# Kernel tuning notes

Measured on AMD Instinct MI355X. Metric: run time of the kernel, lower is better.

Reference implementation:

```python
import jax, jax.numpy as jnp
import numpy as np

L, C, S = 4096, 128, 64
SAMPLE_RATE = 4096.0  # Hz; dt offset is 1/sample_rate as in the flax module


def setup_inputs() -> dict:
    key = jax.random.key(0)
    ks = jax.random.split(key, 4)
    x = jax.random.normal(ks[0], (L, C), dtype=jnp.float32)
    # S4D-real init: A = -arange(1, S+1), param stores log(-A) broadcast to (C, S)
    A_log = jnp.broadcast_to(
        jnp.log(jnp.arange(1, S + 1, dtype=jnp.float32)), (C, S)
    )
    sc = 1.0 / np.sqrt(C)  # lecun_normal-like scale for Dense kernels
    B_kernel = (jax.random.normal(ks[1], (C, S)) * sc).astype(jnp.float32)
    B_bias = jnp.zeros((S,), jnp.float32)
    C_kernel = (jax.random.normal(ks[2], (C, S)) * sc).astype(jnp.float32)
    C_bias = jnp.zeros((S,), jnp.float32)
    dt_kernel = (jax.random.normal(ks[3], (C, C)) * sc).astype(jnp.float32)
    dt_bias = jnp.zeros((C,), jnp.float32)
    return {
        "x": x,
        "A_log": A_log,
        "B_kernel": B_kernel,
        "B_bias": B_bias,
        "C_kernel": C_kernel,
        "C_bias": C_bias,
        "dt_kernel": dt_kernel,
        "dt_bias": dt_bias,
    }


def reference(x, A_log, B_kernel, B_bias, C_kernel, C_bias, dt_kernel, dt_bias):
    # ssm params
    A = -jnp.exp(A_log)                                   # (C, S), negative real
    B = 1.0 + x @ B_kernel + B_bias                       # (L, S)
    Cm = x @ C_kernel + C_bias                            # (L, S)
    dt = jax.nn.softplus(1.0 / SAMPLE_RATE + x @ dt_kernel + dt_bias)  # (L, C)
    # discretization (ZOH for diagonal real A)
    At = jnp.exp(A[None, :, :] * dt[:, :, None])          # (L, C, S)
    ut = (At - 1.0) * (B[:, None, :] / A[None, :, :]) * x[:, :, None]  # (L, C, S)

    # parallel linear-recurrence scan: h_t = At_t * h_{t-1} + ut_t, h0 = 0
    def comb(e1, e2):
        a1, u1 = e1
        a2, u2 = e2
        return (a2 * a1, a2 * u1 + u2)

    _, ht = jax.lax.associative_scan(comb, (At, ut))      # scans over axis 0 (L)
    y = jnp.einsum("ls,lcs->lc", Cm, ht)                  # (L, C)
    return y
```

## Files before the change

### kernel.cpp

```cpp
#include <hip/hip_runtime.h>
#include <math.h>

#define LL 4096
#define CC 128
#define SS 64
#define CLEN 32
#define GW 8
#define NG 16
#define CS 8192

__global__ __launch_bounds__(256) void k_proj(
    const float* __restrict__ x,
    const float* __restrict__ Bk, const float* __restrict__ Bb,
    const float* __restrict__ Ck, const float* __restrict__ Cb,
    const float* __restrict__ Dk, const float* __restrict__ Db,
    float* __restrict__ Bmat, float* __restrict__ Cmat,
    float* __restrict__ DTmT, float* __restrict__ xT)
{
    __shared__ float xs[CC][20];
    const int r0 = blockIdx.x * 16;
    const int t = threadIdx.x;
    {
        const int r = t >> 4, k8 = (t & 15) * 8;
        const float4 v0 = *(const float4*)&x[(r0 + r) * CC + k8];
        const float4 v1 = *(const float4*)&x[(r0 + r) * CC + k8 + 4];
        xs[k8+0][r] = v0.x; xs[k8+1][r] = v0.y; xs[k8+2][r] = v0.z; xs[k8+3][r] = v0.w;
        xs[k8+4][r] = v1.x; xs[k8+5][r] = v1.y; xs[k8+6][r] = v1.z; xs[k8+7][r] = v1.w;
    }
    __syncthreads();
    {
        const int k = t >> 1, half = (t & 1) * 8;
        const float4 a = *(const float4*)&xs[k][half];
        const float4 b = *(const float4*)&xs[k][half + 4];
        *(float4*)&xT[k * LL + r0 + half]     = a;
        *(float4*)&xT[k * LL + r0 + half + 4] = b;
    }
    const int tc = t & 63, tr = t >> 6;
    const float* Wb; int wstride, wo;
    if (tc < 16)      { Wb = Bk; wstride = SS; wo = 4 * tc; }
    else if (tc < 32) { Wb = Ck; wstride = SS; wo = 4 * tc - 64; }
    else              { Wb = Dk; wstride = CC; wo = 4 * tc - 128; }
    float acc[4][4];
#pragma unroll
    for (int r = 0; r < 4; ++r)
#pragma unroll
        for (int j = 0; j < 4; ++j) acc[r][j] = 0.0f;
    for (int k = 0; k < CC; ++k) {
        const float4 wq = *(const float4*)(Wb + k * wstride + wo);
        const float4 xq = *(const float4*)&xs[k][4 * tr];
        const float wv[4] = {wq.x, wq.y, wq.z, wq.w};
        const float xv[4] = {xq.x, xq.y, xq.z, xq.w};
#pragma unroll
        for (int r = 0; r < 4; ++r)
#pragma unroll
            for (int j = 0; j < 4; ++j) acc[r][j] = fmaf(xv[r], wv[j], acc[r][j]);
    }
    const int rb = r0 + 4 * tr;
    if (tc < 32) {
        const float* bb = (tc < 16) ? Bb : Cb;
        const float add = (tc < 16) ? 1.0f : 0.0f;
        float bias[4];
#pragma unroll
        for (int j = 0; j < 4; ++j) bias[j] = add + bb[wo + j];
        float* dst = (tc < 16) ? Bmat : Cmat;
#pragma unroll
        for (int r = 0; r < 4; ++r) {
            const float4 o = make_float4(acc[r][0] + bias[0], acc[r][1] + bias[1],
                                         acc[r][2] + bias[2], acc[r][3] + bias[3]);
            *(float4*)&dst[(rb + r) * SS + wo] = o;
        }
    } else {
#pragma unroll
        for (int j = 0; j < 4; ++j) {
            const float bj = Db[wo + j] + 0.000244140625f;
            float sp[4];
#pragma unroll
            for (int r = 0; r < 4; ++r) {
                const float z = acc[r][j] + bj;
                sp[r] = fmaxf(z, 0.0f) + log1pf(__expf(-fabsf(z)));
            }
            *(float4*)&DTmT[(wo + j) * LL + rb] = make_float4(sp[0], sp[1], sp[2], sp[3]);
        }
    }
}

__global__ __launch_bounds__(512, 4) void k_sweep1(
    const float* __restrict__ xT, const float* __restrict__ A_log,
    const float* __restrict__ Bmat, const float* __restrict__ DTmT,
    float* __restrict__ Ga, float* __restrict__ Gu)
{
    __shared__ float2 agg[GW][SS];
    const int lane = threadIdx.x & 63;
    const int w = __builtin_amdgcn_readfirstlane(threadIdx.x >> 6);
    const int c = blockIdx.x >> 4;
    const int g = blockIdx.x & (NG - 1);
    const int j = c * SS + lane;
    const float A = -__expf(A_log[j]);
    const float invA = 1.0f / A;
    const int l0 = (g * GW + w) * CLEN;
    const float* dtp = DTmT + c * LL + l0;
    const float* xp  = xT   + c * LL + l0;
    const float* Bp  = Bmat + l0 * SS + lane;
    float ap = 1.0f, uc = 0.0f;
#pragma unroll
    for (int i = 0; i < CLEN; ++i) {
        const float At = __expf(A * dtp[i]);
        const float u  = (At - 1.0f) * invA * (Bp[i * SS] * xp[i]);
        ap *= At;
        uc = fmaf(At, uc, u);
    }
    agg[w][lane] = make_float2(ap, uc);
    __syncthreads();
    if (w == 0) {
        float ga = 1.0f, gu = 0.0f;
#pragma unroll
        for (int k = 0; k < GW; ++k) {
            const float2 t = agg[k][lane];
            gu = fmaf(t.x, gu, t.y);
            ga *= t.x;
        }
        Ga[g * CS + j] = ga;
        Gu[g * CS + j] = gu;
    }
}

__global__ __launch_bounds__(512, 4) void k_emit(
    const float* __restrict__ xT, const float* __restrict__ A_log,
    const float* __restrict__ Bmat, const float* __restrict__ Cmat,
    const float* __restrict__ DTmT,
    const float* __restrict__ Ga, const float* __restrict__ Gu,
    float* __restrict__ y)
{
    __shared__ float2 agg[GW][SS];
    const int lane = threadIdx.x & 63;
    const int w = __builtin_amdgcn_readfirstlane(threadIdx.x >> 6);
    const int c = blockIdx.x >> 4;
    const int g = blockIdx.x & (NG - 1);
    const int j = c * SS + lane;
    const float A = -__expf(A_log[j]);
    const float invA = 1.0f / A;
    float hg = 0.0f;
    {
        float gar[NG - 1], gur[NG - 1];
#pragma unroll
        for (int gg = 0; gg < NG - 1; ++gg) {
            gar[gg] = Ga[gg * CS + j];
            gur[gg] = Gu[gg * CS + j];
        }
#pragma unroll
        for (int gg = 0; gg < NG - 1; ++gg)
            hg = (gg < g) ? fmaf(gar[gg], hg, gur[gg]) : hg;
    }
    const int l0 = (g * GW + w) * CLEN;
    const float* dtp = DTmT + c * LL + l0;
    const float* xp  = xT   + c * LL + l0;
    const float* Bp  = Bmat + l0 * SS + lane;
    const float* Cp  = Cmat + l0 * SS + lane;
    float at[CLEN], uu[CLEN];
    {
        float ap = 1.0f, uc = 0.0f;
#pragma unroll
        for (int i = 0; i < CLEN; ++i) {
            at[i] = __expf(A * dtp[i]);
            uu[i] = (at[i] - 1.0f) * invA * (Bp[i * SS] * xp[i]);
            ap *= at[i];
            uc = fmaf(at[i], uc, uu[i]);
        }
        agg[w][lane] = make_float2(ap, uc);
    }
    __syncthreads();
    float ea = 1.0f, eu = 0.0f;
    for (int k = 0; k < w; ++k) {
        const float2 t = agg[k][lane];
        eu = fmaf(t.x, eu, t.y);
        ea *= t.x;
    }
    float h = fmaf(ea, hg, eu);
#pragma unroll
    for (int i = 0; i < CLEN; ++i) {
        h = fmaf(at[i], h, uu[i]);
        uu[i] = Cp[i * SS] * h;
    }
#pragma unroll
    for (int k = 0; k < 5; ++k) {
        const int d = 1 << k;
        const bool hi = (lane & d) != 0;
#pragma unroll
        for (int i2 = 0; i2 < (CLEN >> (k + 1)); ++i2) {
            const float a = uu[2 * i2], b = uu[2 * i2 + 1];
            const float send = hi ? a : b;
            const float t = __shfl_xor(send, d, 64);
            uu[i2] = (hi ? b : a) + t;
        }
    }
    const float t = __shfl_xor(uu[0], 32, 64);
    const float yv = uu[0] + t;
    if (lane < 32) y[(l0 + lane) * CC + c] = yv;
}

extern "C" void kernel_launch(void* const* d_in, const int* in_sizes, int n_in,
                              void* d_out, int out_size, void* d_ws, size_t ws_size,
                              hipStream_t stream)
{
    const float* x  = (const float*)d_in[0];
    const float* Al = (const float*)d_in[1];
    const float* Bk = (const float*)d_in[2];
    const float* Bb = (const float*)d_in[3];
    const float* Ck = (const float*)d_in[4];
    const float* Cb = (const float*)d_in[5];
    const float* Dk = (const float*)d_in[6];
    const float* Db = (const float*)d_in[7];
    float* y  = (float*)d_out;
    float* ws = (float*)d_ws;

    float* Bmat = ws;
    float* Cmat = Bmat + LL * SS;
    float* DTmT = Cmat + LL * SS;
    float* xT   = DTmT + CC * LL;
    float* Ga   = xT   + CC * LL;
    float* Gu   = Ga   + NG * CS;

    k_proj  <<<LL / 16, 256, 0, stream>>>(x, Bk, Bb, Ck, Cb, Dk, Db, Bmat, Cmat, DTmT, xT);
    k_sweep1<<<CC * NG, 512, 0, stream>>>(xT, Al, Bmat, DTmT, Ga, Gu);
    k_emit  <<<CC * NG, 512, 0, stream>>>(xT, Al, Bmat, Cmat, DTmT, Ga, Gu, y);
}
```

Before: 49.83 us.

## Split projection across twice the blocks, use exp2 and pack carry state

The projection kernel now launches twice as many blocks. Each row stripe is split so one block computes the dt projection plus the x transpose, and the other computes the B and C projections, each thread producing two columns instead of four. The scan kernels replace __expf with a hardware exp2 on a pre-scaled A, and store the group carries as interleaved float2 so each load is a single 8-byte access. This is meant to raise parallelism in the projection stage and trim transcendental and load instructions, at the cost of each stripe of x being staged into shared memory twice.

```diff
diff --git a/kernel.cpp b/kernel.cpp
--- a/kernel.cpp
+++ b/kernel.cpp
@@ -8,6 +8,7 @@
 #define GW 8
 #define NG 16
 #define CS 8192
+#define LOG2E 1.44269504088896f
 
 __global__ __launch_bounds__(256) void k_proj(
     const float* __restrict__ x,
@@ -18,7 +19,9 @@
     float* __restrict__ DTmT, float* __restrict__ xT)
 {
     __shared__ float xs[CC][20];
-    const int r0 = blockIdx.x * 16;
+    const int stripe = blockIdx.x >> 1;
+    const int half   = blockIdx.x & 1;
+    const int r0 = stripe * 16;
     const int t = threadIdx.x;
     {
         const int r = t >> 4, k8 = (t & 15) * 8;
@@ -28,58 +31,65 @@
         xs[k8+4][r] = v1.x; xs[k8+5][r] = v1.y; xs[k8+6][r] = v1.z; xs[k8+7][r] = v1.w;
     }
     __syncthreads();
-    {
-        const int k = t >> 1, half = (t & 1) * 8;
-        const float4 a = *(const float4*)&xs[k][half];
-        const float4 b = *(const float4*)&xs[k][half + 4];
-        *(float4*)&xT[k * LL + r0 + half]     = a;
-        *(float4*)&xT[k * LL + r0 + half + 4] = b;
-    }
     const int tc = t & 63, tr = t >> 6;
-    const float* Wb; int wstride, wo;
-    if (tc < 16)      { Wb = Bk; wstride = SS; wo = 4 * tc; }
-    else if (tc < 32) { Wb = Ck; wstride = SS; wo = 4 * tc - 64; }
-    else              { Wb = Dk; wstride = CC; wo = 4 * tc - 128; }
-    float acc[4][4];
-#pragma unroll
-    for (int r = 0; r < 4; ++r)
-#pragma unroll
-        for (int j = 0; j < 4; ++j) acc[r][j] = 0.0f;
-    for (int k = 0; k < CC; ++k) {
-        const float4 wq = *(const float4*)(Wb + k * wstride + wo);
-        const float4 xq = *(const float4*)&xs[k][4 * tr];
-        const float wv[4] = {wq.x, wq.y, wq.z, wq.w};
-        const float xv[4] = {xq.x, xq.y, xq.z, xq.w};
-#pragma unroll
-        for (int r = 0; r < 4; ++r)
-#pragma unroll
-            for (int j = 0; j < 4; ++j) acc[r][j] = fmaf(xv[r], wv[j], acc[r][j]);
-    }
+    const int c2 = 2 * tc;
     const int rb = r0 + 4 * tr;
-    if (tc < 32) {
-        const float* bb = (tc < 16) ? Bb : Cb;
-        const float add = (tc < 16) ? 1.0f : 0.0f;
-        float bias[4];
-#pragma unroll
-        for (int j = 0; j < 4; ++j) bias[j] = add + bb[wo + j];
-        float* dst = (tc < 16) ? Bmat : Cmat;
-#pragma unroll
-        for (int r = 0; r < 4; ++r) {
-            const float4 o = make_float4(acc[r][0] + bias[0], acc[r][1] + bias[1],
-                                         acc[r][2] + bias[2], acc[r][3] + bias[3]);
-            *(float4*)&dst[(rb + r) * SS + wo] = o;
-        }
-    } else {
-#pragma unroll
-        for (int j = 0; j < 4; ++j) {
-            const float bj = Db[wo + j] + 0.000244140625f;
+    if (half == 1) {
+        const int k = t >> 1, h8 = (t & 1) * 8;
+        const float4 a = *(const float4*)&xs[k][h8];
+        const float4 b = *(const float4*)&xs[k][h8 + 4];
+        *(float4*)&xT[k * LL + r0 + h8]     = a;
+        *(float4*)&xT[k * LL + r0 + h8 + 4] = b;
+        float acc[4][2];
+#pragma unroll
+        for (int r = 0; r < 4; ++r) { acc[r][0] = 0.f; acc[r][1] = 0.f; }
+        const float* W = Dk + c2;
+        for (int k2 = 0; k2 < CC; ++k2) {
+            const float2 wq = *(const float2*)(W + k2 * CC);
+            const float4 xq = *(const float4*)&xs[k2][4 * tr];
+            const float xv[4] = {xq.x, xq.y, xq.z, xq.w};
+#pragma unroll
+            for (int r = 0; r < 4; ++r) {
+                acc[r][0] = fmaf(xv[r], wq.x, acc[r][0]);
+                acc[r][1] = fmaf(xv[r], wq.y, acc[r][1]);
+            }
+        }
+#pragma unroll
+        for (int j = 0; j < 2; ++j) {
+            const float bj = Db[c2 + j] + 0.000244140625f;
             float sp[4];
 #pragma unroll
             for (int r = 0; r < 4; ++r) {
                 const float z = acc[r][j] + bj;
                 sp[r] = fmaxf(z, 0.0f) + log1pf(__expf(-fabsf(z)));
             }
-            *(float4*)&DTmT[(wo + j) * LL + rb] = make_float4(sp[0], sp[1], sp[2], sp[3]);
+            *(float4*)&DTmT[(c2 + j) * LL + rb] = make_float4(sp[0], sp[1], sp[2], sp[3]);
+        }
+    } else {
+        const bool isB = (c2 < 64);
+        const int wo = isB ? c2 : (c2 - 64);
+        const float* W = (isB ? Bk : Ck) + wo;
+        const float add = isB ? 1.0f : 0.0f;
+        const float* bb = isB ? Bb : Cb;
+        float* dst = isB ? Bmat : Cmat;
+        float acc[4][2];
+#pragma unroll
+        for (int r = 0; r < 4; ++r) { acc[r][0] = 0.f; acc[r][1] = 0.f; }
+        for (int k2 = 0; k2 < CC; ++k2) {
+            const float2 wq = *(const float2*)(W + k2 * SS);
+            const float4 xq = *(const float4*)&xs[k2][4 * tr];
+            const float xv[4] = {xq.x, xq.y, xq.z, xq.w};
+#pragma unroll
+            for (int r = 0; r < 4; ++r) {
+                acc[r][0] = fmaf(xv[r], wq.x, acc[r][0]);
+                acc[r][1] = fmaf(xv[r], wq.y, acc[r][1]);
+            }
+        }
+        const float b0 = add + bb[wo], b1 = add + bb[wo + 1];
+#pragma unroll
+        for (int r = 0; r < 4; ++r) {
+            const float2 o = make_float2(acc[r][0] + b0, acc[r][1] + b1);
+            *(float2*)&dst[(rb + r) * SS + wo] = o;
         }
     }
 }
@@ -87,7 +97,7 @@
 __global__ __launch_bounds__(512, 4) void k_sweep1(
     const float* __restrict__ xT, const float* __restrict__ A_log,
     const float* __restrict__ Bmat, const float* __restrict__ DTmT,
-    float* __restrict__ Ga, float* __restrict__ Gu)
+    float2* __restrict__ GaGu)
 {
     __shared__ float2 agg[GW][SS];
     const int lane = threadIdx.x & 63;
@@ -96,6 +106,7 @@
     const int g = blockIdx.x & (NG - 1);
     const int j = c * SS + lane;
     const float A = -__expf(A_log[j]);
+    const float A2 = A * LOG2E;
     const float invA = 1.0f / A;
     const int l0 = (g * GW + w) * CLEN;
     const float* dtp = DTmT + c * LL + l0;
@@ -104,7 +115,7 @@
     float ap = 1.0f, uc = 0.0f;
 #pragma unroll
     for (int i = 0; i < CLEN; ++i) {
-        const float At = __expf(A * dtp[i]);
+        const float At = __builtin_amdgcn_exp2f(A2 * dtp[i]);
         const float u  = (At - 1.0f) * invA * (Bp[i * SS] * xp[i]);
         ap *= At;
         uc = fmaf(At, uc, u);
@@ -119,8 +130,7 @@
             gu = fmaf(t.x, gu, t.y);
             ga *= t.x;
         }
-        Ga[g * CS + j] = ga;
-        Gu[g * CS + j] = gu;
+        GaGu[g * CS + j] = make_float2(ga, gu);
     }
 }
 
@@ -128,7 +138,7 @@
     const float* __restrict__ xT, const float* __restrict__ A_log,
     const float* __restrict__ Bmat, const float* __restrict__ Cmat,
     const float* __restrict__ DTmT,
-    const float* __restrict__ Ga, const float* __restrict__ Gu,
+    const float2* __restrict__ GaGu,
     float* __restrict__ y)
 {
     __shared__ float2 agg[GW][SS];
@@ -138,18 +148,16 @@
     const int g = blockIdx.x & (NG - 1);
     const int j = c * SS + lane;
     const float A = -__expf(A_log[j]);
+    const float A2 = A * LOG2E;
     const float invA = 1.0f / A;
     float hg = 0.0f;
     {
-        float gar[NG - 1], gur[NG - 1];
-#pragma unroll
-        for (int gg = 0; gg < NG - 1; ++gg) {
-            gar[gg] = Ga[gg * CS + j];
-            gur[gg] = Gu[gg * CS + j];
-        }
+        float2 ggr[NG - 1];
+#pragma unroll
+        for (int gg = 0; gg < NG - 1; ++gg) ggr[gg] = GaGu[gg * CS + j];
 #pragma unroll
         for (int gg = 0; gg < NG - 1; ++gg)
-            hg = (gg < g) ? fmaf(gar[gg], hg, gur[gg]) : hg;
+            hg = (gg < g) ? fmaf(ggr[gg].x, hg, ggr[gg].y) : hg;
     }
     const int l0 = (g * GW + w) * CLEN;
     const float* dtp = DTmT + c * LL + l0;
@@ -161,7 +169,7 @@
         float ap = 1.0f, uc = 0.0f;
 #pragma unroll
         for (int i = 0; i < CLEN; ++i) {
-            at[i] = __expf(A * dtp[i]);
+            at[i] = __builtin_amdgcn_exp2f(A2 * dtp[i]);
             uu[i] = (at[i] - 1.0f) * invA * (Bp[i * SS] * xp[i]);
             ap *= at[i];
             uc = fmaf(at[i], uc, uu[i]);
@@ -213,14 +221,13 @@
     float* y  = (float*)d_out;
     float* ws = (float*)d_ws;
 
-    float* Bmat = ws;
-    float* Cmat = Bmat + LL * SS;
-    float* DTmT = Cmat + LL * SS;
-    float* xT   = DTmT + CC * LL;
-    float* Ga   = xT   + CC * LL;
-    float* Gu   = Ga   + NG * CS;
-
-    k_proj  <<<LL / 16, 256, 0, stream>>>(x, Bk, Bb, Ck, Cb, Dk, Db, Bmat, Cmat, DTmT, xT);
-    k_sweep1<<<CC * NG, 512, 0, stream>>>(xT, Al, Bmat, DTmT, Ga, Gu);
-    k_emit  <<<CC * NG, 512, 0, stream>>>(xT, Al, Bmat, Cmat, DTmT, Ga, Gu, y);
-}
+    float*  Bmat = ws;
+    float*  Cmat = Bmat + LL * SS;
+    float*  DTmT = Cmat + LL * SS;
+    float*  xT   = DTmT + CC * LL;
+    float2* GaGu = (float2*)(xT + CC * LL);
+
+    k_proj  <<<2 * (LL / 16), 256, 0, stream>>>(x, Bk, Bb, Ck, Cb, Dk, Db, Bmat, Cmat, DTmT, xT);
+    k_sweep1<<<CC * NG,       512, 0, stream>>>(xT, Al, Bmat, DTmT, GaGu);
+    k_emit  <<<CC * NG,       512, 0, stream>>>(xT, Al, Bmat, Cmat, DTmT, GaGu, y);
+}
```

Result: slower. 51.77 us (+3.9%).

## Fuse sweep and emit kernels with decoupled inter-block flag-based prefix passing

Applied to the files above, without the earlier changes.

Merges the two scan kernels into one. Each block publishes its group aggregate to global memory behind a release fence and a flag, then spin-waits on the flags of the earlier groups for the same channel before composing its carry-in. This removes a full second pass over dt, x and B plus a kernel launch. In exchange it adds a memset, a spin-wait whose progress depends on the scheduler running earlier blocks first, and extra latency for later groups. It also switches the exponential to exp2 with a pre-scaled A.

```diff
diff --git a/kernel.cpp b/kernel.cpp
--- a/kernel.cpp
+++ b/kernel.cpp
@@ -8,6 +8,7 @@
 #define GW 8
 #define NG 16
 #define CS 8192
+#define LOG2E 1.44269504088896f
 
 __global__ __launch_bounds__(256) void k_proj(
     const float* __restrict__ x,
@@ -84,73 +85,23 @@
     }
 }
 
-__global__ __launch_bounds__(512, 4) void k_sweep1(
+__global__ __launch_bounds__(512, 4) void k_fused(
     const float* __restrict__ xT, const float* __restrict__ A_log,
-    const float* __restrict__ Bmat, const float* __restrict__ DTmT,
-    float* __restrict__ Ga, float* __restrict__ Gu)
+    const float* __restrict__ Bmat, const float* __restrict__ Cmat,
+    const float* __restrict__ DTmT,
+    float2* __restrict__ GaGu, int* __restrict__ flags,
+    float* __restrict__ y)
 {
     __shared__ float2 agg[GW][SS];
+    __shared__ float hgs[SS];
     const int lane = threadIdx.x & 63;
     const int w = __builtin_amdgcn_readfirstlane(threadIdx.x >> 6);
     const int c = blockIdx.x >> 4;
     const int g = blockIdx.x & (NG - 1);
     const int j = c * SS + lane;
     const float A = -__expf(A_log[j]);
+    const float A2 = A * LOG2E;
     const float invA = 1.0f / A;
-    const int l0 = (g * GW + w) * CLEN;
-    const float* dtp = DTmT + c * LL + l0;
-    const float* xp  = xT   + c * LL + l0;
-    const float* Bp  = Bmat + l0 * SS + lane;
-    float ap = 1.0f, uc = 0.0f;
-#pragma unroll
-    for (int i = 0; i < CLEN; ++i) {
-        const float At = __expf(A * dtp[i]);
-        const float u  = (At - 1.0f) * invA * (Bp[i * SS] * xp[i]);
-        ap *= At;
-        uc = fmaf(At, uc, u);
-    }
-    agg[w][lane] = make_float2(ap, uc);
-    __syncthreads();
-    if (w == 0) {
-        float ga = 1.0f, gu = 0.0f;
-#pragma unroll
-        for (int k = 0; k < GW; ++k) {
-            const float2 t = agg[k][lane];
-            gu = fmaf(t.x, gu, t.y);
-            ga *= t.x;
-        }
-        Ga[g * CS + j] = ga;
-        Gu[g * CS + j] = gu;
-    }
-}
-
-__global__ __launch_bounds__(512, 4) void k_emit(
-    const float* __restrict__ xT, const float* __restrict__ A_log,
-    const float* __restrict__ Bmat, const float* __restrict__ Cmat,
-    const float* __restrict__ DTmT,
-    const float* __restrict__ Ga, const float* __restrict__ Gu,
-    float* __restrict__ y)
-{
-    __shared__ float2 agg[GW][SS];
-    const int lane = threadIdx.x & 63;
-    const int w = __builtin_amdgcn_readfirstlane(threadIdx.x >> 6);
-    const int c = blockIdx.x >> 4;
-    const int g = blockIdx.x & (NG - 1);
-    const int j = c * SS + lane;
-    const float A = -__expf(A_log[j]);
-    const float invA = 1.0f / A;
-    float hg = 0.0f;
-    {
-        float gar[NG - 1], gur[NG - 1];
-#pragma unroll
-        for (int gg = 0; gg < NG - 1; ++gg) {
-            gar[gg] = Ga[gg * CS + j];
-            gur[gg] = Gu[gg * CS + j];
-        }
-#pragma unroll
-        for (int gg = 0; gg < NG - 1; ++gg)
-            hg = (gg < g) ? fmaf(gar[gg], hg, gur[gg]) : hg;
-    }
     const int l0 = (g * GW + w) * CLEN;
     const float* dtp = DTmT + c * LL + l0;
     const float* xp  = xT   + c * LL + l0;
@@ -161,7 +112,7 @@
         float ap = 1.0f, uc = 0.0f;
 #pragma unroll
         for (int i = 0; i < CLEN; ++i) {
-            at[i] = __expf(A * dtp[i]);
+            at[i] = __builtin_amdgcn_exp2f(A2 * dtp[i]);
             uu[i] = (at[i] - 1.0f) * invA * (Bp[i * SS] * xp[i]);
             ap *= at[i];
             uc = fmaf(at[i], uc, uu[i]);
@@ -169,6 +120,43 @@
         agg[w][lane] = make_float2(ap, uc);
     }
     __syncthreads();
+    if (w == 0) {
+        float ga = 1.0f, gu = 0.0f;
+#pragma unroll
+        for (int k = 0; k < GW; ++k) {
+            const float2 t = agg[k][lane];
+            gu = fmaf(t.x, gu, t.y);
+            ga *= t.x;
+        }
+        if (g < NG - 1) {
+            GaGu[g * CS + j] = make_float2(ga, gu);
+            __builtin_amdgcn_fence(__ATOMIC_RELEASE, "agent");
+            if (lane == 0)
+                __hip_atomic_store(&flags[c * NG + g], 1,
+                                   __ATOMIC_RELAXED, __HIP_MEMORY_SCOPE_AGENT);
+        }
+        float hg = 0.0f;
+        if (g > 0) {
+            for (;;) {
+                int f = (lane < g)
+                    ? __hip_atomic_load(&flags[c * NG + lane],
+                                        __ATOMIC_RELAXED, __HIP_MEMORY_SCOPE_AGENT)
+                    : 1;
+                if (__all(f != 0)) break;
+                __builtin_amdgcn_s_sleep(1);
+            }
+            __builtin_amdgcn_fence(__ATOMIC_ACQUIRE, "agent");
+            float2 ggr[NG - 1];
+#pragma unroll
+            for (int gg = 0; gg < NG - 1; ++gg) ggr[gg] = GaGu[gg * CS + j];
+#pragma unroll
+            for (int gg = 0; gg < NG - 1; ++gg)
+                hg = (gg < g) ? fmaf(ggr[gg].x, hg, ggr[gg].y) : hg;
+        }
+        hgs[lane] = hg;
+    }
+    __syncthreads();
+    const float hg = hgs[lane];
     float ea = 1.0f, eu = 0.0f;
     for (int k = 0; k < w; ++k) {
         const float2 t = agg[k][lane];
@@ -213,14 +201,14 @@
     float* y  = (float*)d_out;
     float* ws = (float*)d_ws;
 
-    float* Bmat = ws;
-    float* Cmat = Bmat + LL * SS;
-    float* DTmT = Cmat + LL * SS;
-    float* xT   = DTmT + CC * LL;
-    float* Ga   = xT   + CC * LL;
-    float* Gu   = Ga   + NG * CS;
-
-    k_proj  <<<LL / 16, 256, 0, stream>>>(x, Bk, Bb, Ck, Cb, Dk, Db, Bmat, Cmat, DTmT, xT);
-    k_sweep1<<<CC * NG, 512, 0, stream>>>(xT, Al, Bmat, DTmT, Ga, Gu);
-    k_emit  <<<CC * NG, 512, 0, stream>>>(xT, Al, Bmat, Cmat, DTmT, Ga, Gu, y);
+    float*  Bmat = ws;
+    float*  Cmat = Bmat + LL * SS;
+    float*  DTmT = Cmat + LL * SS;
+    float*  xT   = DTmT + CC * LL;
+    float2* GaGu = (float2*)(xT + CC * LL);
+    int*    flags = (int*)(GaGu + NG * CS);
+
+    hipMemsetAsync(flags, 0, CC * NG * sizeof(int), stream);
+    k_proj <<<LL / 16, 256, 0, stream>>>(x, Bk, Bb, Ck, Cb, Dk, Db, Bmat, Cmat, DTmT, xT);
+    k_fused<<<CC * NG, 512, 0, stream>>>(xT, Al, Bmat, Cmat, DTmT, GaGu, flags, y);
 }
```

After: 112.3 us. +125.3%, slower.
